# Performance work log

Hardware: AMD Instinct MI355X
Metric: run time of the kernel (lower is better)

The kernel has to match this reference:

```python
import jax, jax.numpy as jnp
import numpy as np

D_K = 64  # head dim used for scaling, matches init d_k


def setup_inputs() -> dict:
    key = jax.random.key(0)
    k1, k2, k3 = jax.random.split(key, 3)
    shape = (2, 2048, 16, 64)  # [batch, seq, heads, head_dim]
    q = jax.random.normal(k1, shape, dtype=jnp.float32)
    k = jax.random.normal(k2, shape, dtype=jnp.float32)
    v = jax.random.normal(k3, shape, dtype=jnp.float32)
    return {"q": q, "k": k, "v": v}


def reference(q, k, v):
    # score: [n, h, q, k]
    scale = 1.0 / np.sqrt(D_K).astype(np.float32)
    score = jnp.einsum('nqhd,nkhd->nhqk', q, k) * scale
    attn = jax.nn.softmax(score, axis=-1)
    context = jnp.einsum('nhqk,nkhd->nqhd', attn, v)
    return (context, attn)
```

## Files before the change

kernel.cpp:

```cpp
#include <hip/hip_runtime.h>

#define BATCH 2
#define SEQ   2048
#define NH    16
#define HD    64
#define RS    (NH*HD)
#define NPAIR (BATCH*NH)
#define NKT   (SEQ/64)
#define TILE_SHORTS 4096

typedef float f32x4  __attribute__((ext_vector_type(4)));
typedef short short8 __attribute__((ext_vector_type(8)));

#define GAS __attribute__((address_space(1)))
#define LAS __attribute__((address_space(3)))

__device__ __forceinline__ unsigned f2bf(float f) {
    union { float f; unsigned u; } c; c.f = f;
    return (c.u + 0x7FFFu + ((c.u >> 16) & 1u)) >> 16;
}
__device__ __forceinline__ unsigned pk(float lo, float hi) {
    return f2bf(lo) | (f2bf(hi) << 16);
}
__device__ __forceinline__ int swz(int row, int bc) {
    return (row * 128 + bc) ^ ((row & 7) << 4);
}
__device__ __forceinline__ short8 ld16(const void* p) {
    union { uint4 u; short8 s; } cv;
    cv.u = *(const uint4*)p;
    return cv.s;
}

extern "C" __global__ __launch_bounds__(256)
void pack_kv(const float* __restrict__ k, const float* __restrict__ v,
             unsigned short* __restrict__ ktl, unsigned short* __restrict__ vtl)
{
    __shared__ float Vf[64 * 65];
    const int bid = blockIdx.x;
    const int tid = threadIdx.x;

    if (bid < NPAIR * NKT) {
        const int kti = bid & 31, h = (bid >> 5) & 15, n = bid >> 9;
        const float* Kg = k + (((long)n * SEQ + kti * 64) * NH + h) * HD;
        uint4* out = (uint4*)(ktl + (long)bid * TILE_SHORTS);
        #pragma unroll
        for (int i = 0; i < 2; ++i) {
            int cidx = tid + i * 256;
            int c = cidx >> 7, j = (cidx >> 6) & 1, l = cidx & 63;
            const float* src = Kg + (c * 16 + (l & 15)) * RS + j * 32 + (l >> 4) * 8;
            float4 f0 = *(const float4*)src;
            float4 f1 = *(const float4*)(src + 4);
            uint4 o = { pk(f0.x, f0.y), pk(f0.z, f0.w), pk(f1.x, f1.y), pk(f1.z, f1.w) };
            out[cidx] = o;
        }
    } else {
        const int b2 = bid - NPAIR * NKT;
        const int kti = b2 & 31, h = (b2 >> 5) & 15, n = b2 >> 9;
        const float* Vg = v + (((long)n * SEQ + kti * 64) * NH + h) * HD;
        #pragma unroll
        for (int i = 0; i < 4; ++i) {
            int idx = tid + i * 256;
            int row = idx >> 4, c4 = idx & 15;
            float4 f = *(const float4*)(Vg + row * RS + c4 * 4);
            Vf[row * 65 + c4 * 4 + 0] = f.x;
            Vf[row * 65 + c4 * 4 + 1] = f.y;
            Vf[row * 65 + c4 * 4 + 2] = f.z;
            Vf[row * 65 + c4 * 4 + 3] = f.w;
        }
        __syncthreads();
        uint4* out = (uint4*)(vtl + (long)b2 * TILE_SHORTS);
        #pragma unroll
        for (int i = 0; i < 2; ++i) {
            int cidx = tid + i * 256;
            int c = cidx >> 7, j = (cidx >> 6) & 1, l = cidx & 63;
            int d = c * 16 + (l & 15);
            int kb = j * 32 + (l >> 4) * 8;
            float a0 = Vf[(kb + 0) * 65 + d], a1 = Vf[(kb + 1) * 65 + d];
            float a2 = Vf[(kb + 2) * 65 + d], a3 = Vf[(kb + 3) * 65 + d];
            float a4 = Vf[(kb + 4) * 65 + d], a5 = Vf[(kb + 5) * 65 + d];
            float a6 = Vf[(kb + 6) * 65 + d], a7 = Vf[(kb + 7) * 65 + d];
            uint4 o = { pk(a0, a1), pk(a2, a3), pk(a4, a5), pk(a6, a7) };
            out[cidx] = o;
        }
    }
}

extern "C" __global__ __launch_bounds__(256, 4)
void sdpa_kernel(const float* __restrict__ q,
                 const unsigned short* __restrict__ ktl,
                 const unsigned short* __restrict__ vtl,
                 float* __restrict__ ctx, float* __restrict__ attn,
                 int skip_pair)
{
    __shared__ unsigned short Kd[2][TILE_SHORTS];
    __shared__ unsigned short Vd[2][TILE_SHORTS];
    __shared__ unsigned short Ps[4][1024];

    const int bid0 = blockIdx.x;
    const int bid  = ((bid0 & 7) << 7) | (bid0 >> 3);
    const int qt = bid & 31, pair = bid >> 5;
    const int h = pair & 15, n = pair >> 4;
    const int tid = threadIdx.x;
    const int w = tid >> 6, lane = tid & 63, lh = lane & 15, ks = lane >> 4;
    const bool wattn = (pair != skip_pair);

    const float* Qr = q + (((long)n * SEQ + qt * 64 + w * 16 + lh) * NH + h) * HD;
    short8 bq0, bq1;
    {
        union { unsigned u[4]; short8 s; } t;
        float4 f0 = *(const float4*)(Qr + ks * 8);
        float4 f1 = *(const float4*)(Qr + ks * 8 + 4);
        t.u[0] = pk(f0.x * 0.125f, f0.y * 0.125f);
        t.u[1] = pk(f0.z * 0.125f, f0.w * 0.125f);
        t.u[2] = pk(f1.x * 0.125f, f1.y * 0.125f);
        t.u[3] = pk(f1.z * 0.125f, f1.w * 0.125f);
        bq0 = t.s;
        float4 g0 = *(const float4*)(Qr + 32 + ks * 8);
        float4 g1 = *(const float4*)(Qr + 32 + ks * 8 + 4);
        t.u[0] = pk(g0.x * 0.125f, g0.y * 0.125f);
        t.u[1] = pk(g0.z * 0.125f, g0.w * 0.125f);
        t.u[2] = pk(g1.x * 0.125f, g1.y * 0.125f);
        t.u[3] = pk(g1.z * 0.125f, g1.w * 0.125f);
        bq1 = t.s;
    }

    const unsigned short* Ktile = ktl + (long)pair * NKT * TILE_SHORTS;
    const unsigned short* Vtile = vtl + (long)pair * NKT * TILE_SHORTS;

    auto stage = [&](unsigned short* lbuf, const unsigned short* gt) {
        #pragma unroll
        for (int i = 0; i < 2; ++i) {
            const unsigned short* g = gt + w * 1024 + i * 512 + lane * 8;
            unsigned short* l = lbuf + w * 1024 + i * 512;
            __builtin_amdgcn_global_load_lds((const GAS unsigned int*)g,
                                             (LAS unsigned int*)l, 16, 0, 0);
        }
    };

    float lsum = 0.f;
    #pragma unroll 2
    for (int kt = 0; kt < NKT; ++kt) {
        const char* T = (const char*)(Ktile + (long)kt * TILE_SHORTS);
        #pragma unroll
        for (int c = 0; c < 4; ++c) {
            short8 a0 = ld16(T + ((c * 2 + 0) * 64 + lane) * 16);
            short8 a1 = ld16(T + ((c * 2 + 1) * 64 + lane) * 16);
            f32x4 z = {0.f, 0.f, 0.f, 0.f};
            z = __builtin_amdgcn_mfma_f32_16x16x32_bf16(a0, bq0, z, 0, 0, 0);
            z = __builtin_amdgcn_mfma_f32_16x16x32_bf16(a1, bq1, z, 0, 0, 0);
            lsum += __expf(z[0]) + __expf(z[1]) + __expf(z[2]) + __expf(z[3]);
        }
    }
    lsum += __shfl_xor(lsum, 16);
    lsum += __shfl_xor(lsum, 32);
    const float linv = 1.0f / lsum;

    f32x4 oacc[4];
    #pragma unroll
    for (int cd = 0; cd < 4; ++cd) oacc[cd] = (f32x4){0.f, 0.f, 0.f, 0.f};

    float* attnW = attn + (((long)pair) * SEQ + qt * 64 + w * 16 + lh) * SEQ + ks * 4;
    char* Pw = (char*)Ps[w];

    stage(Kd[0], Ktile);
    stage(Vd[0], Vtile);
    asm volatile("s_waitcnt vmcnt(0)" ::: "memory");
    __builtin_amdgcn_s_barrier();

    for (int kt = 0; kt < NKT; ++kt) {
        const int cur = kt & 1;
        if (kt < NKT - 1) {
            stage(Kd[cur ^ 1], Ktile + (kt + 1) * TILE_SHORTS);
            stage(Vd[cur ^ 1], Vtile + (kt + 1) * TILE_SHORTS);
        }
        asm volatile("" ::: "memory");

        const char* Kb = (const char*)Kd[cur];
        f32x4 s[4];
        #pragma unroll
        for (int c = 0; c < 4; ++c) {
            short8 a0 = ld16(Kb + ((c * 2 + 0) * 64 + lane) * 16);
            short8 a1 = ld16(Kb + ((c * 2 + 1) * 64 + lane) * 16);
            f32x4 z = {0.f, 0.f, 0.f, 0.f};
            z = __builtin_amdgcn_mfma_f32_16x16x32_bf16(a0, bq0, z, 0, 0, 0);
            z = __builtin_amdgcn_mfma_f32_16x16x32_bf16(a1, bq1, z, 0, 0, 0);
            s[c] = z;
        }
        #pragma unroll
        for (int c = 0; c < 4; ++c) {
            f32x4 pv;
            pv[0] = __expf(s[c][0]) * linv;
            pv[1] = __expf(s[c][1]) * linv;
            pv[2] = __expf(s[c][2]) * linv;
            pv[3] = __expf(s[c][3]) * linv;
            if (wattn) {
                __builtin_nontemporal_store(pv, (f32x4*)(attnW + (long)kt * 64 + c * 16));
            }
            uint2 u2 = { pk(pv[0], pv[1]), pk(pv[2], pv[3]) };
            *(uint2*)(Pw + swz(lh, c * 32 + ks * 8)) = u2;
        }
        short8 pa0 = ld16(Pw + swz(lh, ks * 16));
        short8 pa1 = ld16(Pw + swz(lh, 64 + ks * 16));
        const char* Vb = (const char*)Vd[cur];
        #pragma unroll
        for (int cd = 0; cd < 4; ++cd) {
            short8 bv0 = ld16(Vb + ((cd * 2 + 0) * 64 + lane) * 16);
            short8 bv1 = ld16(Vb + ((cd * 2 + 1) * 64 + lane) * 16);
            oacc[cd] = __builtin_amdgcn_mfma_f32_16x16x32_bf16(pa0, bv0, oacc[cd], 0, 0, 0);
            oacc[cd] = __builtin_amdgcn_mfma_f32_16x16x32_bf16(pa1, bv1, oacc[cd], 0, 0, 0);
        }
        if (kt < NKT - 1) {
            if (wattn) asm volatile("s_waitcnt vmcnt(4)" ::: "memory");
            else       asm volatile("s_waitcnt vmcnt(0)" ::: "memory");
            __builtin_amdgcn_s_barrier();
        }
    }

    float* ctxW = ctx + (((long)n * SEQ + qt * 64 + w * 16 + ks * 4) * NH + h) * HD + lh;
    #pragma unroll
    for (int cd = 0; cd < 4; ++cd) {
        #pragma unroll
        for (int r = 0; r < 4; ++r) {
            ctxW[r * RS + cd * 16] = oacc[cd][r];
        }
    }
}

extern "C" __global__ __launch_bounds__(256, 4)
void attn_fill(const float* __restrict__ q, const float* __restrict__ k,
               float* __restrict__ attn, int pair)
{
    __shared__ unsigned short Ksh[TILE_SHORTS];
    const int n = pair >> 4, h = pair & 15;
    const int qt = blockIdx.x;
    const int tid = threadIdx.x;
    const int w = tid >> 6, lane = tid & 63, lh = lane & 15, ks = lane >> 4;

    const float* Qr = q + (((long)n * SEQ + qt * 64 + w * 16 + lh) * NH + h) * HD;
    short8 bq0, bq1;
    {
        union { unsigned u[4]; short8 s; } t;
        float4 f0 = *(const float4*)(Qr + ks * 8);
        float4 f1 = *(const float4*)(Qr + ks * 8 + 4);
        t.u[0] = pk(f0.x * 0.125f, f0.y * 0.125f);
        t.u[1] = pk(f0.z * 0.125f, f0.w * 0.125f);
        t.u[2] = pk(f1.x * 0.125f, f1.y * 0.125f);
        t.u[3] = pk(f1.z * 0.125f, f1.w * 0.125f);
        bq0 = t.s;
        float4 g0 = *(const float4*)(Qr + 32 + ks * 8);
        float4 g1 = *(const float4*)(Qr + 32 + ks * 8 + 4);
        t.u[0] = pk(g0.x * 0.125f, g0.y * 0.125f);
        t.u[1] = pk(g0.z * 0.125f, g0.w * 0.125f);
        t.u[2] = pk(g1.x * 0.125f, g1.y * 0.125f);
        t.u[3] = pk(g1.z * 0.125f, g1.w * 0.125f);
        bq1 = t.s;
    }

    const float* Kg = k + ((long)n * SEQ * NH + h) * HD;

    float lsum = 0.f;
    for (int kt = 0; kt < NKT; ++kt) {
        __syncthreads();
        #pragma unroll
        for (int i = 0; i < 2; ++i) {
            int cidx = tid + i * 256;
            int c = cidx >> 7, j = (cidx >> 6) & 1, l = cidx & 63;
            const float* src = Kg + ((long)kt * 64 + c * 16 + (l & 15)) * RS + j * 32 + (l >> 4) * 8;
            float4 f0 = *(const float4*)src;
            float4 f1 = *(const float4*)(src + 4);
            uint4 o = { pk(f0.x, f0.y), pk(f0.z, f0.w), pk(f1.x, f1.y), pk(f1.z, f1.w) };
            *((uint4*)Ksh + cidx) = o;
        }
        __syncthreads();
        #pragma unroll
        for (int c = 0; c < 4; ++c) {
            short8 a0 = ld16((const char*)Ksh + ((c * 2 + 0) * 64 + lane) * 16);
            short8 a1 = ld16((const char*)Ksh + ((c * 2 + 1) * 64 + lane) * 16);
            f32x4 z = {0.f, 0.f, 0.f, 0.f};
            z = __builtin_amdgcn_mfma_f32_16x16x32_bf16(a0, bq0, z, 0, 0, 0);
            z = __builtin_amdgcn_mfma_f32_16x16x32_bf16(a1, bq1, z, 0, 0, 0);
            lsum += __expf(z[0]) + __expf(z[1]) + __expf(z[2]) + __expf(z[3]);
        }
    }
    lsum += __shfl_xor(lsum, 16);
    lsum += __shfl_xor(lsum, 32);
    const float linv = 1.0f / lsum;

    float* attnW = attn + (((long)pair) * SEQ + qt * 64 + w * 16 + lh) * SEQ + ks * 4;
    for (int kt = 0; kt < NKT; ++kt) {
        __syncthreads();
        #pragma unroll
        for (int i = 0; i < 2; ++i) {
            int cidx = tid + i * 256;
            int c = cidx >> 7, j = (cidx >> 6) & 1, l = cidx & 63;
            const float* src = Kg + ((long)kt * 64 + c * 16 + (l & 15)) * RS + j * 32 + (l >> 4) * 8;
            float4 f0 = *(const float4*)src;
            float4 f1 = *(const float4*)(src + 4);
            uint4 o = { pk(f0.x, f0.y), pk(f0.z, f0.w), pk(f1.x, f1.y), pk(f1.z, f1.w) };
            *((uint4*)Ksh + cidx) = o;
        }
        __syncthreads();
        #pragma unroll
        for (int c = 0; c < 4; ++c) {
            short8 a0 = ld16((const char*)Ksh + ((c * 2 + 0) * 64 + lane) * 16);
            short8 a1 = ld16((const char*)Ksh + ((c * 2 + 1) * 64 + lane) * 16);
            f32x4 z = {0.f, 0.f, 0.f, 0.f};
            z = __builtin_amdgcn_mfma_f32_16x16x32_bf16(a0, bq0, z, 0, 0, 0);
            z = __builtin_amdgcn_mfma_f32_16x16x32_bf16(a1, bq1, z, 0, 0, 0);
            f32x4 pv;
            pv[0] = __expf(z[0]) * linv;
            pv[1] = __expf(z[1]) * linv;
            pv[2] = __expf(z[2]) * linv;
            pv[3] = __expf(z[3]) * linv;
            *(f32x4*)(attnW + (long)kt * 64 + c * 16) = pv;
        }
    }
}

extern "C" void kernel_launch(void* const* d_in, const int* in_sizes, int n_in,
                              void* d_out, int out_size, void* d_ws, size_t ws_size,
                              hipStream_t stream)
{
    const float* q = (const float*)d_in[0];
    const float* k = (const float*)d_in[1];
    const float* v = (const float*)d_in[2];
    float* ctx  = (float*)d_out;
    float* attn = ctx + (size_t)BATCH * SEQ * NH * HD;

    const size_t tiles_shorts = (size_t)NPAIR * NKT * TILE_SHORTS;
    const size_t ws_need = 2 * tiles_shorts * sizeof(unsigned short);

    unsigned short *ktl, *vtl;
    int skip;
    if (ws_size >= ws_need) {
        ktl = (unsigned short*)d_ws;
        vtl = ktl + tiles_shorts;
        skip = -1;
    } else {
        ktl = (unsigned short*)(attn + (size_t)(NPAIR - 1) * SEQ * SEQ);
        vtl = ktl + tiles_shorts;
        skip = NPAIR - 1;
    }

    hipLaunchKernelGGL(pack_kv, dim3(2 * NPAIR * NKT), dim3(256), 0, stream, k, v, ktl, vtl);
    hipLaunchKernelGGL(sdpa_kernel, dim3(NPAIR * NKT), dim3(256), 0, stream, q, ktl, vtl, ctx, attn, skip);
    if (skip >= 0) {
        hipLaunchKernelGGL(attn_fill, dim3(32), dim3(256), 0, stream, q, k, attn, skip);
    }
}
```

Before: 208.0 us.

## Stage K into LDS for the row-sum pass and parallelize the fallback attn fill

The first pass that computes softmax row sums now double-buffers packed K tiles into shared memory with global_load_lds and barriers, replacing direct global loads of each tile. When the workspace is too small and one head pair's attention is written by a separate kernel, the main kernel now stores that pair's inverse row sums. A new 1024-block fill kernel then reads them and writes each 64x64 tile independently, replacing the 32-block kernel that redid both passes. This adds barriers to the main kernel's first pass, and the faster fill only runs when the workspace is large enough to hold the inverse row sums but too small for the packed K/V tiles.

```diff
diff --git a/kernel.cpp b/kernel.cpp
--- a/kernel.cpp
+++ b/kernel.cpp
@@ -31,6 +31,37 @@
     return cv.s;
 }
 
+__device__ __forceinline__ void load_qfrag(const float* Qr, int ks, short8& bq0, short8& bq1) {
+    union { unsigned u[4]; short8 s; } t;
+    float4 f0 = *(const float4*)(Qr + ks * 8);
+    float4 f1 = *(const float4*)(Qr + ks * 8 + 4);
+    t.u[0] = pk(f0.x * 0.125f, f0.y * 0.125f);
+    t.u[1] = pk(f0.z * 0.125f, f0.w * 0.125f);
+    t.u[2] = pk(f1.x * 0.125f, f1.y * 0.125f);
+    t.u[3] = pk(f1.z * 0.125f, f1.w * 0.125f);
+    bq0 = t.s;
+    float4 g0 = *(const float4*)(Qr + 32 + ks * 8);
+    float4 g1 = *(const float4*)(Qr + 32 + ks * 8 + 4);
+    t.u[0] = pk(g0.x * 0.125f, g0.y * 0.125f);
+    t.u[1] = pk(g0.z * 0.125f, g0.w * 0.125f);
+    t.u[2] = pk(g1.x * 0.125f, g1.y * 0.125f);
+    t.u[3] = pk(g1.z * 0.125f, g1.w * 0.125f);
+    bq1 = t.s;
+}
+
+__device__ __forceinline__ void stage_k_from_f32(const float* Kt, unsigned short* Ksh, int tid) {
+    #pragma unroll
+    for (int i = 0; i < 2; ++i) {
+        int cidx = tid + i * 256;
+        int c = cidx >> 7, j = (cidx >> 6) & 1, l = cidx & 63;
+        const float* src = Kt + (c * 16 + (l & 15)) * RS + j * 32 + (l >> 4) * 8;
+        float4 f0 = *(const float4*)src;
+        float4 f1 = *(const float4*)(src + 4);
+        uint4 o = { pk(f0.x, f0.y), pk(f0.z, f0.w), pk(f1.x, f1.y), pk(f1.z, f1.w) };
+        *((uint4*)Ksh + cidx) = o;
+    }
+}
+
 extern "C" __global__ __launch_bounds__(256)
 void pack_kv(const float* __restrict__ k, const float* __restrict__ v,
              unsigned short* __restrict__ ktl, unsigned short* __restrict__ vtl)
@@ -42,17 +73,7 @@
     if (bid < NPAIR * NKT) {
         const int kti = bid & 31, h = (bid >> 5) & 15, n = bid >> 9;
         const float* Kg = k + (((long)n * SEQ + kti * 64) * NH + h) * HD;
-        uint4* out = (uint4*)(ktl + (long)bid * TILE_SHORTS);
-        #pragma unroll
-        for (int i = 0; i < 2; ++i) {
-            int cidx = tid + i * 256;
-            int c = cidx >> 7, j = (cidx >> 6) & 1, l = cidx & 63;
-            const float* src = Kg + (c * 16 + (l & 15)) * RS + j * 32 + (l >> 4) * 8;
-            float4 f0 = *(const float4*)src;
-            float4 f1 = *(const float4*)(src + 4);
-            uint4 o = { pk(f0.x, f0.y), pk(f0.z, f0.w), pk(f1.x, f1.y), pk(f1.z, f1.w) };
-            out[cidx] = o;
-        }
+        stage_k_from_f32(Kg, ktl + (long)bid * TILE_SHORTS, tid);
     } else {
         const int b2 = bid - NPAIR * NKT;
         const int kti = b2 & 31, h = (b2 >> 5) & 15, n = b2 >> 9;
@@ -90,7 +111,7 @@
                  const unsigned short* __restrict__ ktl,
                  const unsigned short* __restrict__ vtl,
                  float* __restrict__ ctx, float* __restrict__ attn,
-                 int skip_pair)
+                 float* __restrict__ linv_out, int skip_pair)
 {
     __shared__ unsigned short Kd[2][TILE_SHORTS];
     __shared__ unsigned short Vd[2][TILE_SHORTS];
@@ -106,23 +127,7 @@
 
     const float* Qr = q + (((long)n * SEQ + qt * 64 + w * 16 + lh) * NH + h) * HD;
     short8 bq0, bq1;
-    {
-        union { unsigned u[4]; short8 s; } t;
-        float4 f0 = *(const float4*)(Qr + ks * 8);
-        float4 f1 = *(const float4*)(Qr + ks * 8 + 4);
-        t.u[0] = pk(f0.x * 0.125f, f0.y * 0.125f);
-        t.u[1] = pk(f0.z * 0.125f, f0.w * 0.125f);
-        t.u[2] = pk(f1.x * 0.125f, f1.y * 0.125f);
-        t.u[3] = pk(f1.z * 0.125f, f1.w * 0.125f);
-        bq0 = t.s;
-        float4 g0 = *(const float4*)(Qr + 32 + ks * 8);
-        float4 g1 = *(const float4*)(Qr + 32 + ks * 8 + 4);
-        t.u[0] = pk(g0.x * 0.125f, g0.y * 0.125f);
-        t.u[1] = pk(g0.z * 0.125f, g0.w * 0.125f);
-        t.u[2] = pk(g1.x * 0.125f, g1.y * 0.125f);
-        t.u[3] = pk(g1.z * 0.125f, g1.w * 0.125f);
-        bq1 = t.s;
-    }
+    load_qfrag(Qr, ks, bq0, bq1);
 
     const unsigned short* Ktile = ktl + (long)pair * NKT * TILE_SHORTS;
     const unsigned short* Vtile = vtl + (long)pair * NKT * TILE_SHORTS;
@@ -137,23 +142,33 @@
         }
     };
 
+    stage(Kd[0], Ktile);
+    asm volatile("s_waitcnt vmcnt(0)" ::: "memory");
+    __builtin_amdgcn_s_barrier();
     float lsum = 0.f;
-    #pragma unroll 2
     for (int kt = 0; kt < NKT; ++kt) {
-        const char* T = (const char*)(Ktile + (long)kt * TILE_SHORTS);
-        #pragma unroll
-        for (int c = 0; c < 4; ++c) {
-            short8 a0 = ld16(T + ((c * 2 + 0) * 64 + lane) * 16);
-            short8 a1 = ld16(T + ((c * 2 + 1) * 64 + lane) * 16);
+        const int cur = kt & 1;
+        if (kt < NKT - 1) stage(Kd[cur ^ 1], Ktile + (kt + 1) * TILE_SHORTS);
+        const char* Kb = (const char*)Kd[cur];
+        #pragma unroll
+        for (int c = 0; c < 4; ++c) {
+            short8 a0 = ld16(Kb + ((c * 2 + 0) * 64 + lane) * 16);
+            short8 a1 = ld16(Kb + ((c * 2 + 1) * 64 + lane) * 16);
             f32x4 z = {0.f, 0.f, 0.f, 0.f};
             z = __builtin_amdgcn_mfma_f32_16x16x32_bf16(a0, bq0, z, 0, 0, 0);
             z = __builtin_amdgcn_mfma_f32_16x16x32_bf16(a1, bq1, z, 0, 0, 0);
             lsum += __expf(z[0]) + __expf(z[1]) + __expf(z[2]) + __expf(z[3]);
         }
+        asm volatile("s_waitcnt vmcnt(0)" ::: "memory");
+        __builtin_amdgcn_s_barrier();
     }
     lsum += __shfl_xor(lsum, 16);
     lsum += __shfl_xor(lsum, 32);
     const float linv = 1.0f / lsum;
+
+    if (pair == skip_pair && linv_out && ks == 0) {
+        linv_out[qt * 64 + w * 16 + lh] = linv;
+    }
 
     f32x4 oacc[4];
     #pragma unroll
@@ -226,9 +241,46 @@
     }
 }
 
+extern "C" __global__ __launch_bounds__(256)
+void attn_fill_fast(const float* __restrict__ q, const float* __restrict__ k,
+                    float* __restrict__ attn, const float* __restrict__ linv_in,
+                    int pair)
+{
+    __shared__ unsigned short Ksh[TILE_SHORTS];
+    const int n = pair >> 4, h = pair & 15;
+    const int qt = blockIdx.x & 31, kt = blockIdx.x >> 5;
+    const int tid = threadIdx.x;
+    const int w = tid >> 6, lane = tid & 63, lh = lane & 15, ks = lane >> 4;
+
+    const float* Qr = q + (((long)n * SEQ + qt * 64 + w * 16 + lh) * NH + h) * HD;
+    short8 bq0, bq1;
+    load_qfrag(Qr, ks, bq0, bq1);
+    const float linv = linv_in[qt * 64 + w * 16 + lh];
+
+    const float* Kt = k + (((long)n * SEQ + kt * 64) * NH + h) * HD;
+    stage_k_from_f32(Kt, Ksh, tid);
+    __syncthreads();
+
+    float* attnW = attn + (((long)pair) * SEQ + qt * 64 + w * 16 + lh) * SEQ + ks * 4;
+    #pragma unroll
+    for (int c = 0; c < 4; ++c) {
+        short8 a0 = ld16((const char*)Ksh + ((c * 2 + 0) * 64 + lane) * 16);
+        short8 a1 = ld16((const char*)Ksh + ((c * 2 + 1) * 64 + lane) * 16);
+        f32x4 z = {0.f, 0.f, 0.f, 0.f};
+        z = __builtin_amdgcn_mfma_f32_16x16x32_bf16(a0, bq0, z, 0, 0, 0);
+        z = __builtin_amdgcn_mfma_f32_16x16x32_bf16(a1, bq1, z, 0, 0, 0);
+        f32x4 pv;
+        pv[0] = __expf(z[0]) * linv;
+        pv[1] = __expf(z[1]) * linv;
+        pv[2] = __expf(z[2]) * linv;
+        pv[3] = __expf(z[3]) * linv;
+        __builtin_nontemporal_store(pv, (f32x4*)(attnW + (long)kt * 64 + c * 16));
+    }
+}
+
 extern "C" __global__ __launch_bounds__(256, 4)
-void attn_fill(const float* __restrict__ q, const float* __restrict__ k,
-               float* __restrict__ attn, int pair)
+void attn_fill_slow(const float* __restrict__ q, const float* __restrict__ k,
+                    float* __restrict__ attn, int pair)
 {
     __shared__ unsigned short Ksh[TILE_SHORTS];
     const int n = pair >> 4, h = pair & 15;
@@ -238,39 +290,14 @@
 
     const float* Qr = q + (((long)n * SEQ + qt * 64 + w * 16 + lh) * NH + h) * HD;
     short8 bq0, bq1;
-    {
-        union { unsigned u[4]; short8 s; } t;
-        float4 f0 = *(const float4*)(Qr + ks * 8);
-        float4 f1 = *(const float4*)(Qr + ks * 8 + 4);
-        t.u[0] = pk(f0.x * 0.125f, f0.y * 0.125f);
-        t.u[1] = pk(f0.z * 0.125f, f0.w * 0.125f);
-        t.u[2] = pk(f1.x * 0.125f, f1.y * 0.125f);
-        t.u[3] = pk(f1.z * 0.125f, f1.w * 0.125f);
-        bq0 = t.s;
-        float4 g0 = *(const float4*)(Qr + 32 + ks * 8);
-        float4 g1 = *(const float4*)(Qr + 32 + ks * 8 + 4);
-        t.u[0] = pk(g0.x * 0.125f, g0.y * 0.125f);
-        t.u[1] = pk(g0.z * 0.125f, g0.w * 0.125f);
-        t.u[2] = pk(g1.x * 0.125f, g1.y * 0.125f);
-        t.u[3] = pk(g1.z * 0.125f, g1.w * 0.125f);
-        bq1 = t.s;
-    }
+    load_qfrag(Qr, ks, bq0, bq1);
 
     const float* Kg = k + ((long)n * SEQ * NH + h) * HD;
 
     float lsum = 0.f;
     for (int kt = 0; kt < NKT; ++kt) {
         __syncthreads();
-        #pragma unroll
-        for (int i = 0; i < 2; ++i) {
-            int cidx = tid + i * 256;
-            int c = cidx >> 7, j = (cidx >> 6) & 1, l = cidx & 63;
-            const float* src = Kg + ((long)kt * 64 + c * 16 + (l & 15)) * RS + j * 32 + (l >> 4) * 8;
-            float4 f0 = *(const float4*)src;
-            float4 f1 = *(const float4*)(src + 4);
-            uint4 o = { pk(f0.x, f0.y), pk(f0.z, f0.w), pk(f1.x, f1.y), pk(f1.z, f1.w) };
-            *((uint4*)Ksh + cidx) = o;
-        }
+        stage_k_from_f32(Kg + (long)kt * 64 * RS, Ksh, tid);
         __syncthreads();
         #pragma unroll
         for (int c = 0; c < 4; ++c) {
@@ -289,16 +316,7 @@
     float* attnW = attn + (((long)pair) * SEQ + qt * 64 + w * 16 + lh) * SEQ + ks * 4;
     for (int kt = 0; kt < NKT; ++kt) {
         __syncthreads();
-        #pragma unroll
-        for (int i = 0; i < 2; ++i) {
-            int cidx = tid + i * 256;
-            int c = cidx >> 7, j = (cidx >> 6) & 1, l = cidx & 63;
-            const float* src = Kg + ((long)kt * 64 + c * 16 + (l & 15)) * RS + j * 32 + (l >> 4) * 8;
-            float4 f0 = *(const float4*)src;
-            float4 f1 = *(const float4*)(src + 4);
-            uint4 o = { pk(f0.x, f0.y), pk(f0.z, f0.w), pk(f1.x, f1.y), pk(f1.z, f1.w) };
-            *((uint4*)Ksh + cidx) = o;
-        }
+        stage_k_from_f32(Kg + (long)kt * 64 * RS, Ksh, tid);
         __syncthreads();
         #pragma unroll
         for (int c = 0; c < 4; ++c) {
@@ -342,9 +360,18 @@
         skip = NPAIR - 1;
     }
 
+    const bool linv_fits = (ws_size >= SEQ * sizeof(float));
+    float* linv_ws = (skip >= 0 && linv_fits) ? (float*)d_ws : nullptr;
+
     hipLaunchKernelGGL(pack_kv, dim3(2 * NPAIR * NKT), dim3(256), 0, stream, k, v, ktl, vtl);
-    hipLaunchKernelGGL(sdpa_kernel, dim3(NPAIR * NKT), dim3(256), 0, stream, q, ktl, vtl, ctx, attn, skip);
+    hipLaunchKernelGGL(sdpa_kernel, dim3(NPAIR * NKT), dim3(256), 0, stream,
+                       q, ktl, vtl, ctx, attn, linv_ws, skip);
     if (skip >= 0) {
-        hipLaunchKernelGGL(attn_fill, dim3(32), dim3(256), 0, stream, q, k, attn, skip);
-    }
-}
+        if (linv_ws) {
+            hipLaunchKernelGGL(attn_fill_fast, dim3(NKT * 32), dim3(256), 0, stream,
+                               q, k, attn, linv_ws, skip);
+        } else {
+            hipLaunchKernelGGL(attn_fill_slow, dim3(32), dim3(256), 0, stream, q, k, attn, skip);
+        }
+    }
+}
```

New measurement: 208.6 us. About the same (+0.3%).
